# Kernel tuning notes

Measured on AMD Instinct MI355X. Metric: run time of the kernel, lower is better.

The kernel has to match this reference:

```python
import jax, jax.numpy as jnp
import numpy as np

B, L, D, H = 4, 2048, 512, 8
HD = D // H
NEG = -1e9


def setup_inputs() -> dict:
    key = jax.random.key(0)
    ks = jax.random.split(key, 11)
    s = 1.0 / np.sqrt(D)
    inp = {
        "q": jax.random.normal(ks[0], (B, L, D), jnp.float32),
        "k": jax.random.normal(ks[1], (B, L, D), jnp.float32),
        "v": jax.random.normal(ks[2], (B, L, D), jnp.float32),
        "mask": jnp.broadcast_to(jnp.tril(jnp.ones((L, L), jnp.int32)), (B, L, L)),
        "Wq": jax.random.normal(ks[3], (D, D), jnp.float32) * s,
        "bq": jax.random.normal(ks[4], (D,), jnp.float32) * s,
        "Wk": jax.random.normal(ks[5], (D, D), jnp.float32) * s,
        "bk": jax.random.normal(ks[6], (D,), jnp.float32) * s,
        "Wv": jax.random.normal(ks[7], (D, D), jnp.float32) * s,
        "bv": jax.random.normal(ks[8], (D,), jnp.float32) * s,
        "Wo": jax.random.normal(ks[9], (D, D), jnp.float32) * s,
        "bo": jax.random.normal(ks[10], (D,), jnp.float32) * s,
    }
    return inp


def reference(q, k, v, mask, Wq, bq, Wk, bk, Wv, bv, Wo, bo):
    # Linear projections (torch Linear: x @ W.T + b)
    Q = (q @ Wq.T + bq).reshape(B, L, H, HD).transpose(0, 2, 1, 3)  # [B,H,L,hd]
    K = (k @ Wk.T + bk).reshape(B, L, H, HD).transpose(0, 2, 1, 3)
    V = (v @ Wv.T + bv).reshape(B, L, H, HD).transpose(0, 2, 1, 3)
    # scaled dot-product attention with masked_fill(mask==0, -1e9)
    score = jnp.einsum('bhqd,bhkd->bhqk', Q, K) / jnp.sqrt(jnp.float32(HD))
    score = jnp.where(mask[:, None, :, :] == 0, NEG, score)
    attn = jax.nn.softmax(score, axis=-1)
    ctx = jnp.einsum('bhqk,bhkd->bhqd', attn, V)  # [B,H,L,hd]
    ctx = ctx.transpose(0, 2, 1, 3).reshape(B, L, D)
    return ctx @ Wo.T + bo
```

## Files before the change

### kernel.cpp

```cpp
#include <hip/hip_runtime.h>
#include <hip/hip_bf16.h>
#include <math.h>

constexpr int Bc  = 4;
constexpr int Lc  = 2048;
constexpr int Dc  = 512;
constexpr int Hc  = 8;
constexpr int HDc = 64;

constexpr int GK = Dc;
constexpr int BK = 64;

typedef __attribute__((ext_vector_type(8))) short bf16x8;
typedef __attribute__((ext_vector_type(4))) short bf16x4;
typedef __attribute__((ext_vector_type(4))) float f32x4;
typedef __attribute__((ext_vector_type(16))) float f32x16;
typedef __attribute__((ext_vector_type(4))) int i32x4;

static __device__ __forceinline__ short f2bf(float x) {
    __hip_bfloat16 h = __float2bfloat16(x);
    return (short)__builtin_bit_cast(unsigned short, h);
}

static __device__ __forceinline__ int cvtpk_bf16(float lo, float hi) {
    int r;
    asm("v_cvt_pk_bf16_f32 %0, %1, %2" : "=v"(r) : "v"(lo), "v"(hi));
    return r;
}

static __device__ __forceinline__ void gload_lds16(const void* g, void* l) {
    __builtin_amdgcn_global_load_lds(
        (const __attribute__((address_space(1))) void*)g,
        (__attribute__((address_space(3))) void*)l, 16, 0, 0);
}

__global__ __launch_bounds__(256)
void cast_all(const float* __restrict__ q, const float* __restrict__ k,
              const float* __restrict__ v, const float* __restrict__ wq,
              const float* __restrict__ wk, const float* __restrict__ wv,
              const float* __restrict__ wo, short* __restrict__ dst) {
    const size_t i = ((size_t)blockIdx.x * 256 + threadIdx.x) * 8;
    const float* src; size_t off;
    if      (i <  4194304) { src = q;  off = i; }
    else if (i <  8388608) { src = k;  off = i -  4194304; }
    else if (i < 12582912) { src = v;  off = i -  8388608; }
    else if (i < 12845056) { src = wq; off = i - 12582912; }
    else if (i < 13107200) { src = wk; off = i - 12845056; }
    else if (i < 13369344) { src = wv; off = i - 13107200; }
    else                   { src = wo; off = i - 13369344; }
    const float4 a = *(const float4*)(src + off);
    const float4 b = *(const float4*)(src + off + 4);
    bf16x8 o;
    o[0] = f2bf(a.x); o[1] = f2bf(a.y); o[2] = f2bf(a.z); o[3] = f2bf(a.w);
    o[4] = f2bf(b.x); o[5] = f2bf(b.y); o[6] = f2bf(b.z); o[7] = f2bf(b.w);
    *(bf16x8*)(dst + i) = o;
}

template<int BM, int BN, int WMT, int WNT>
__device__ __forceinline__ void gemm_tile(const short* __restrict__ A,
                                          const short* __restrict__ W,
                                          short* As, short* Bs,
                                          f32x4 (&acc)[WMT][WNT],
                                          int m0, int n0) {
    const int tid  = threadIdx.x;
    const int w    = tid >> 6;
    const int lane = tid & 63;
    const int low4 = lane & 15;
    const int quad = lane >> 4;
    const int wm   = w & 1, wn = w >> 1;
    const int lrow = lane >> 3;
    const int lchk = (lane & 7) * 8;

    for (int k0 = 0; k0 < GK; k0 += BK) {
#pragma unroll
        for (int i = 0; i < BM / 32; ++i) {
            const int r0 = i * 32 + w * 8;
            gload_lds16(A + (size_t)(m0 + r0 + lrow) * GK + k0 + lchk, As + r0 * BK);
        }
#pragma unroll
        for (int i = 0; i < BN / 32; ++i) {
            const int r0 = i * 32 + w * 8;
            gload_lds16(W + (size_t)(n0 + r0 + lrow) * GK + k0 + lchk, Bs + r0 * BK);
        }
        __syncthreads();
#pragma unroll
        for (int ks = 0; ks < 2; ++ks) {
            bf16x8 af[WMT], bfr[WNT];
#pragma unroll
            for (int mi = 0; mi < WMT; ++mi)
                af[mi] = *(const bf16x8*)(As + (wm * WMT * 16 + mi * 16 + low4) * BK + ks * 32 + quad * 8);
#pragma unroll
            for (int ni = 0; ni < WNT; ++ni)
                bfr[ni] = *(const bf16x8*)(Bs + (wn * WNT * 16 + ni * 16 + low4) * BK + ks * 32 + quad * 8);
#pragma unroll
            for (int mi = 0; mi < WMT; ++mi)
#pragma unroll
                for (int ni = 0; ni < WNT; ++ni)
                    acc[mi][ni] = __builtin_amdgcn_mfma_f32_16x16x32_bf16(af[mi], bfr[ni], acc[mi][ni], 0, 0, 0);
        }
        __syncthreads();
    }
}

__global__ __launch_bounds__(256)
void qkv_gemm(const short* __restrict__ Xq, const short* __restrict__ Xk,
              const short* __restrict__ Xv, const short* __restrict__ Wcat,
              const float* __restrict__ bq, const float* __restrict__ bk,
              const float* __restrict__ bv,
              short* __restrict__ Qw, short* __restrict__ Kw, short* __restrict__ Vw) {
    __shared__ __align__(16) short Smem[128 * 138];
    short* As = Smem;
    short* Bs = Smem + 8192;
    short* Ts = Smem;

    const int tid = threadIdx.x;
    const int i    = blockIdx.x;
    const int slot = i >> 3;
    const int g    = (i & 7) + 8 * (slot >> 2);
    const int j    = slot & 3;
    const int z    = g >> 6;
    const int m0   = (g & 63) * 128;
    const int n0   = z * 512 + j * 128;

    const short* A    = (z == 0) ? Xq : (z == 1) ? Xk : Xv;
    const float* bias = (z == 0) ? bq : (z == 1) ? bk : bv;

    f32x4 acc[4][4];
#pragma unroll
    for (int mi = 0; mi < 4; ++mi)
#pragma unroll
        for (int ni = 0; ni < 4; ++ni) acc[mi][ni] = (f32x4){0.f, 0.f, 0.f, 0.f};

    gemm_tile<128, 128, 4, 4>(A, Wcat, As, Bs, acc, m0, n0);

    const int lane = tid & 63, w = tid >> 6;
    const int low4 = lane & 15, quad = lane >> 4;
    const int wm = w & 1, wn = w >> 1;

    if (z < 2) {
        short* Y = (z == 0) ? Qw : Kw;
        const float qs = (z == 0) ? 0.18033688f : 1.0f;
#pragma unroll
        for (int mi = 0; mi < 4; ++mi)
#pragma unroll
            for (int ni = 0; ni < 4; ++ni)
#pragma unroll
                for (int r = 0; r < 4; ++r) {
                    const int rowL = wm * 64 + mi * 16 + quad * 4 + r;
                    const int colL = wn * 64 + ni * 16 + low4;
                    const int c    = (n0 & 511) + colL;
                    Ts[rowL * 138 + colL] = f2bf((acc[mi][ni][r] + bias[c]) * qs);
                }
        __syncthreads();
        const int jj = tid & 7;
        const int b = m0 >> 11;
#pragma unroll
        for (int it = 0; it < 8; ++it) {
            const int slot2 = it * 32 + (tid >> 3);
            const int row  = slot2 >> 1, half = slot2 & 1;
            const int c0 = (n0 & 511) + half * 64;
            const int h  = c0 >> 6;
            const int l  = (m0 & 2047) + row;
            short* dst = Y + (((size_t)b * Hc + h) * Lc + l) * HDc + jj * 8;
            *(bf16x8*)dst = *(const bf16x8*)(Ts + row * 138 + half * 64 + jj * 8);
        }
    } else {
#pragma unroll
        for (int mi = 0; mi < 4; ++mi)
#pragma unroll
            for (int ni = 0; ni < 4; ++ni)
#pragma unroll
                for (int r = 0; r < 4; ++r) {
                    const int rowL = wm * 64 + mi * 16 + quad * 4 + r;
                    const int colL = wn * 64 + ni * 16 + low4;
                    const int c    = (n0 + colL) & 511;
                    Ts[colL * 136 + rowL] = f2bf(acc[mi][ni][r] + bias[c]);
                }
        __syncthreads();
        const int hdl = tid >> 1, seg = tid & 1;
        const int c  = (n0 + hdl) & 511;
        const int h  = c >> 6, hd = c & 63;
        const int b  = m0 >> 11, l0 = (m0 & 2047) + seg * 64;
        short* dst = Vw + (((size_t)b * Hc + h) * HDc + hd) * Lc + l0;
        const short* srcT = Ts + hdl * 136 + seg * 64;
#pragma unroll
        for (int jj = 0; jj < 8; ++jj)
            *(bf16x8*)(dst + jj * 8) = *(const bf16x8*)(srcT + jj * 8);
    }
}

__global__ __launch_bounds__(256)
void out_gemm(const short* __restrict__ A, const short* __restrict__ W,
              const float* __restrict__ bias, float* __restrict__ Y) {
    __shared__ __align__(16) float SmemF[64 * 132];
    short* As = (short*)SmemF;
    short* Bs = As + 64 * BK;
    float* Tf = SmemF;

    const int tid = threadIdx.x;
    const int i    = blockIdx.x;
    const int slot = i >> 3;
    const int g    = (i & 7) + 8 * (slot >> 2);
    const int j    = slot & 3;
    const int m0   = g * 64;
    const int n0   = j * 128;

    f32x4 acc[2][4];
#pragma unroll
    for (int mi = 0; mi < 2; ++mi)
#pragma unroll
        for (int ni = 0; ni < 4; ++ni) acc[mi][ni] = (f32x4){0.f, 0.f, 0.f, 0.f};

    gemm_tile<64, 128, 2, 4>(A, W, As, Bs, acc, m0, n0);

    const int lane = tid & 63, w = tid >> 6;
    const int low4 = lane & 15, quad = lane >> 4;
    const int wm = w & 1, wn = w >> 1;
#pragma unroll
    for (int mi = 0; mi < 2; ++mi)
#pragma unroll
        for (int ni = 0; ni < 4; ++ni)
#pragma unroll
            for (int r = 0; r < 4; ++r) {
                const int rowL = wm * 32 + mi * 16 + quad * 4 + r;
                const int colL = wn * 64 + ni * 16 + low4;
                Tf[rowL * 132 + colL] = acc[mi][ni][r] + bias[n0 + colL];
            }
    __syncthreads();

    const int c = (tid & 31) * 4;
#pragma unroll
    for (int p = 0; p < 8; ++p) {
        const int row = p * 8 + (tid >> 5);
        *(float4*)(Y + (size_t)(m0 + row) * Dc + n0 + c) =
            *(const float4*)(Tf + row * 132 + c);
    }
}

__global__ __launch_bounds__(256, 4)
void flash_attn(const short* __restrict__ Qb, const short* __restrict__ Kb,
                const short* __restrict__ VTb, short* __restrict__ ctx) {
    __shared__ __align__(16) short Kf[2][4096];
    __shared__ __align__(16) short Vf[2][4096];

    const int tid  = threadIdx.x;
    const int w    = tid >> 6;
    const int lane = tid & 63;
    const int t31  = lane & 31;
    const int hh   = lane >> 5;
    const int x7   = t31 & 7;
    const int qcol = w & 1;
    const int kh   = w >> 1;

    const int u  = blockIdx.x;
    const int bh = u & 31;
    const int j  = u >> 5;
    const int a  = (j < 16) ? (31 - j) : (j - 16);
    const int n  = a + 1;
    const int q0 = a * 64 + qcol * 32;

    const short* Qg = Qb  + (size_t)bh * Lc * HDc;
    const short* Kg = Kb  + (size_t)bh * Lc * HDc;
    const short* Vg = VTb + (size_t)bh * HDc * Lc;

    const int grow = lane >> 3;
    const int gcol = ((lane & 7) ^ grow) * 8;

    const int bb = bh >> 3, head = bh & 7;
    short* cg = ctx + (size_t)bb * Lc * Dc + (size_t)head * HDc;

#define STAGE(KT_, BUF_)                                                       \
    {                                                                          \
        _Pragma("unroll")                                                      \
        for (int p = 0; p < 2; ++p) {                                          \
            const int ii = w + 4 * p;                                          \
            gload_lds16(Kg + (size_t)((KT_) + ii * 8 + grow) * HDc + gcol,     \
                        &Kf[BUF_][ii * 512]);                                  \
            gload_lds16(Vg + (size_t)(ii * 8 + grow) * Lc + (KT_) + gcol,      \
                        &Vf[BUF_][ii * 512]);                                  \
        }                                                                      \
    }

    bf16x8 qa[4];
#pragma unroll
    for (int hc = 0; hc < 4; ++hc)
        qa[hc] = *(const bf16x8*)(Qg + (size_t)(q0 + t31) * HDc + hc * 16 + hh * 8);

    STAGE(0, 0);
    asm volatile("s_waitcnt vmcnt(0)" ::: "memory");
    __builtin_amdgcn_sched_barrier(0);
    __builtin_amdgcn_s_barrier();

    f32x16 o0, o1;
#pragma unroll
    for (int i = 0; i < 16; ++i) { o0[i] = 0.f; o1[i] = 0.f; }
    float lps = 0.f;

    for (int t = 0; t < n; ++t) {
        const int buf = t & 1;
        if (t + 1 < n) STAGE((t + 1) * 64, buf ^ 1);

        const bool lastT = (t == a);
        if (!(lastT && qcol == 0 && kh == 1)) {
            f32x16 s;
#pragma unroll
            for (int i = 0; i < 16; ++i) s[i] = 0.f;
            const short* kfb = Kf[buf];
#pragma unroll
            for (int hc = 0; hc < 4; ++hc) {
                const int cb = ((hc * 2 + hh) ^ x7) << 3;
                const bf16x8 kfr = *(const bf16x8*)(kfb + (kh * 32 + t31) * 64 + cb);
                s = __builtin_amdgcn_mfma_f32_32x32x16_bf16(kfr, qa[hc], s, 0, 0, 0);
            }

            if (lastT && !(qcol == 1 && kh == 0)) {
                const int qv  = q0 + t31;
                const int kb0 = t * 64 + kh * 32 + 4 * hh;
#pragma unroll
                for (int r = 0; r < 16; ++r) {
                    const int kl = kb0 + (r & 3) + 8 * (r >> 2);
                    const float p = (kl <= qv) ? exp2f(s[r]) : 0.f;
                    lps += p; s[r] = p;
                }
            } else {
#pragma unroll
                for (int r = 0; r < 16; ++r) {
                    const float p = exp2f(s[r]);
                    lps += p; s[r] = p;
                }
            }

            const short* vfb = Vf[buf];
#pragma unroll
            for (int kc = 0; kc < 2; ++kc) {
                const int g = 8 * kc;
                int u0 = cvtpk_bf16(s[g],     s[g + 1]);
                int u1 = cvtpk_bf16(s[g + 2], s[g + 3]);
                int v0 = cvtpk_bf16(s[g + 4], s[g + 5]);
                int v1 = cvtpk_bf16(s[g + 6], s[g + 7]);
                asm volatile("v_permlane32_swap_b32 %0, %1" : "+v"(u0), "+v"(v0));
                asm volatile("v_permlane32_swap_b32 %0, %1" : "+v"(u1), "+v"(v1));
                i32x4 pw; pw[0] = u0; pw[1] = u1; pw[2] = v0; pw[3] = v1;
                const bf16x8 pa = __builtin_bit_cast(bf16x8, pw);

                const int cbv = ((kh * 4 + kc * 2 + hh) ^ x7) << 3;
                const bf16x8 vf0 = *(const bf16x8*)(vfb + t31 * 64 + cbv);
                const bf16x8 vf1 = *(const bf16x8*)(vfb + (32 + t31) * 64 + cbv);
                o0 = __builtin_amdgcn_mfma_f32_32x32x16_bf16(pa, vf0, o0, 0, 0, 0);
                o1 = __builtin_amdgcn_mfma_f32_32x32x16_bf16(pa, vf1, o1, 0, 0, 0);
            }
        }

        asm volatile("s_waitcnt vmcnt(0)" ::: "memory");
        __builtin_amdgcn_sched_barrier(0);
        __builtin_amdgcn_s_barrier();
    }

    lps += __shfl_xor(lps, 32, 64);

    float* CbX = (qcol == 0) ? (float*)&Kf[1][0] : (float*)&Vf[1][0];
    float* ClX = (float*)&Kf[0][0] + qcol * 64;

    if (kh == 1) {
#pragma unroll
        for (int jj = 0; jj < 4; ++jj) {
            f32x4 a0 = {o0[4 * jj], o0[4 * jj + 1], o0[4 * jj + 2], o0[4 * jj + 3]};
            f32x4 a1 = {o1[4 * jj], o1[4 * jj + 1], o1[4 * jj + 2], o1[4 * jj + 3]};
            *(f32x4*)&CbX[lane * 32 + jj * 4]      = a0;
            *(f32x4*)&CbX[lane * 32 + 16 + jj * 4] = a1;
        }
        ClX[lane] = lps;
    }
    __syncthreads();
    if (kh == 0) {
        lps += ClX[lane];
#pragma unroll
        for (int jj = 0; jj < 4; ++jj) {
            const f32x4 a0 = *(const f32x4*)&CbX[lane * 32 + jj * 4];
            const f32x4 a1 = *(const f32x4*)&CbX[lane * 32 + 16 + jj * 4];
#pragma unroll
            for (int e = 0; e < 4; ++e) {
                o0[4 * jj + e] += a0[e];
                o1[4 * jj + e] += a1[e];
            }
        }
        const float inv = 1.f / lps;
#pragma unroll
        for (int r = 0; r < 16; ++r) {
            const int qloc = (r & 3) + 8 * (r >> 2) + 4 * hh;
            const float iq = __shfl(inv, qloc, 64);
            short* row = cg + (size_t)(q0 + qloc) * Dc;
            row[t31]      = f2bf(o0[r] * iq);
            row[32 + t31] = f2bf(o1[r] * iq);
        }
    }
#undef STAGE
}

extern "C" void kernel_launch(void* const* d_in, const int* in_sizes, int n_in,
                              void* d_out, int out_size, void* d_ws, size_t ws_size,
                              hipStream_t stream) {
    const float* q  = (const float*)d_in[0];
    const float* k  = (const float*)d_in[1];
    const float* v  = (const float*)d_in[2];
    const float* Wq = (const float*)d_in[4];
    const float* bq = (const float*)d_in[5];
    const float* Wk = (const float*)d_in[6];
    const float* bk = (const float*)d_in[7];
    const float* Wv = (const float*)d_in[8];
    const float* bv = (const float*)d_in[9];
    const float* Wo = (const float*)d_in[10];
    const float* bo = (const float*)d_in[11];
    float* out = (float*)d_out;

    const size_t per = (size_t)Bc * Lc * Dc;
    const size_t wsz = (size_t)Dc * Dc;
    short* Xq   = (short*)d_ws;
    short* Xk   = Xq + per;
    short* Xv   = Xk + per;
    short* Wcat = Xv + per;
    short* Wob  = Wcat + 3 * wsz;
    short* Qw   = Wob + wsz;
    short* Kw   = Qw + per;
    short* Vw   = Kw + per;
    short* Cw   = Vw + per;

    cast_all<<<6656, 256, 0, stream>>>(q, k, v, Wq, Wk, Wv, Wo, Xq);

    qkv_gemm<<<768, 256, 0, stream>>>(Xq, Xk, Xv, Wcat,
                                      bq, bk, bv, Qw, Kw, Vw);

    flash_attn<<<1024, 256, 0, stream>>>(Qw, Kw, Vw, Cw);

    out_gemm<<<512, 256, 0, stream>>>(Cw, Wob, bo, out);
}
```

Measured before the change: 223.0 us.

## Split long causal query tiles across two blocks with atomic-counter merge

The flash attention grid grows from 1024 to 1536 blocks. Query tiles 16-31 with the longest causal key ranges are each split into two halves of KV tiles. Each half writes unnormalized partial O and row sums to a workspace, and the second block to finish (chosen with an atomic counter) merges them and writes the normalized output. The goal is to balance load and shorten the tail from the longest tiles. In exchange it adds fp32 workspace traffic, threadfences, an atomic, and a memset launch.

```diff
diff --git a/kernel.cpp b/kernel.cpp
--- a/kernel.cpp
+++ b/kernel.cpp
@@ -239,7 +239,9 @@
 
 __global__ __launch_bounds__(256, 4)
 void flash_attn(const short* __restrict__ Qb, const short* __restrict__ Kb,
-                const short* __restrict__ VTb, short* __restrict__ ctx) {
+                const short* __restrict__ VTb, short* __restrict__ ctx,
+                float* __restrict__ Ows, float* __restrict__ Lws,
+                int* __restrict__ cnt) {
     __shared__ __align__(16) short Kf[2][4096];
     __shared__ __align__(16) short Vf[2][4096];
 
@@ -254,9 +256,24 @@
 
     const int u  = blockIdx.x;
     const int bh = u & 31;
-    const int j  = u >> 5;
-    const int a  = (j < 16) ? (31 - j) : (j - 16);
-    const int n  = a + 1;
+    const int e  = u >> 5;
+
+    int a, t0, t1, c;
+    bool split;
+    if (e < 32) {
+        a = 31 - (e >> 1);
+        const int n = a + 1;
+        const int h = (n + 1) >> 1;
+        c  = e & 1;
+        t0 = c ? h : 0;
+        t1 = c ? n : h;
+        split = true;
+    } else {
+        a = 47 - e;
+        c = 0; t0 = 0; t1 = a + 1;
+        split = false;
+    }
+    const int nt = t1 - t0;
     const int q0 = a * 64 + qcol * 32;
 
     const short* Qg = Qb  + (size_t)bh * Lc * HDc;
@@ -286,7 +303,7 @@
     for (int hc = 0; hc < 4; ++hc)
         qa[hc] = *(const bf16x8*)(Qg + (size_t)(q0 + t31) * HDc + hc * 16 + hh * 8);
 
-    STAGE(0, 0);
+    STAGE(t0 * 64, 0);
     asm volatile("s_waitcnt vmcnt(0)" ::: "memory");
     __builtin_amdgcn_sched_barrier(0);
     __builtin_amdgcn_s_barrier();
@@ -296,11 +313,12 @@
     for (int i = 0; i < 16; ++i) { o0[i] = 0.f; o1[i] = 0.f; }
     float lps = 0.f;
 
-    for (int t = 0; t < n; ++t) {
+    for (int t = 0; t < nt; ++t) {
         const int buf = t & 1;
-        if (t + 1 < n) STAGE((t + 1) * 64, buf ^ 1);
-
-        const bool lastT = (t == a);
+        const int tg  = t0 + t;
+        if (t + 1 < nt) STAGE((tg + 1) * 64, buf ^ 1);
+
+        const bool lastT = (tg == a);
         if (!(lastT && qcol == 0 && kh == 1)) {
             f32x16 s;
 #pragma unroll
@@ -315,7 +333,7 @@
 
             if (lastT && !(qcol == 1 && kh == 0)) {
                 const int qv  = q0 + t31;
-                const int kb0 = t * 64 + kh * 32 + 4 * hh;
+                const int kb0 = tg * 64 + kh * 32 + 4 * hh;
 #pragma unroll
                 for (int r = 0; r < 16; ++r) {
                     const int kl = kb0 + (r & 3) + 8 * (r >> 2);
@@ -358,8 +376,9 @@
 
     lps += __shfl_xor(lps, 32, 64);
 
-    float* CbX = (qcol == 0) ? (float*)&Kf[1][0] : (float*)&Vf[1][0];
-    float* ClX = (float*)&Kf[0][0] + qcol * 64;
+    float* CbX  = (qcol == 0) ? (float*)&Kf[1][0] : (float*)&Vf[1][0];
+    float* ClX  = (float*)&Kf[0][0] + qcol * 64;
+    int* flagp  = (int*)&Kf[0][0] + 192;
 
     if (kh == 1) {
 #pragma unroll
@@ -379,11 +398,49 @@
             const f32x4 a0 = *(const f32x4*)&CbX[lane * 32 + jj * 4];
             const f32x4 a1 = *(const f32x4*)&CbX[lane * 32 + 16 + jj * 4];
 #pragma unroll
-            for (int e = 0; e < 4; ++e) {
-                o0[4 * jj + e] += a0[e];
-                o1[4 * jj + e] += a1[e];
-            }
-        }
+            for (int ee = 0; ee < 4; ++ee) {
+                o0[4 * jj + ee] += a0[ee];
+                o1[4 * jj + ee] += a1[ee];
+            }
+        }
+    }
+
+    if (!split) {
+        if (kh == 0) {
+            const float inv = 1.f / lps;
+#pragma unroll
+            for (int r = 0; r < 16; ++r) {
+                const int qloc = (r & 3) + 8 * (r >> 2) + 4 * hh;
+                const float iq = __shfl(inv, qloc, 64);
+                short* row = cg + (size_t)(q0 + qloc) * Dc;
+                row[t31]      = f2bf(o0[r] * iq);
+                row[32 + t31] = f2bf(o1[r] * iq);
+            }
+        }
+        return;
+    }
+
+    const int slot = (bh << 4) | (a - 16);
+    if (kh == 0) {
+        float* dst = Ows + ((size_t)(slot * 2 + c) << 12) + qcol * 2048 + lane * 32;
+#pragma unroll
+        for (int r = 0; r < 16; ++r) { dst[r] = o0[r]; dst[16 + r] = o1[r]; }
+        if (hh == 0) Lws[(slot * 2 + c) * 64 + qcol * 32 + t31] = lps;
+    }
+    __threadfence();
+    __syncthreads();
+    if (tid == 0) *flagp = atomicAdd(&cnt[slot], 1);
+    __syncthreads();
+    if (*flagp == 0) return;
+
+    __threadfence();
+    if (kh == 0) {
+        const float* Po = Ows + ((size_t)(slot * 2 + (1 - c)) << 12)
+                        + qcol * 2048 + lane * 32;
+#pragma unroll
+        for (int r = 0; r < 16; ++r) { o0[r] += Po[r]; o1[r] += Po[16 + r]; }
+        lps += Lws[(slot * 2 + (1 - c)) * 64 + qcol * 32 + t31];
+
         const float inv = 1.f / lps;
 #pragma unroll
         for (int r = 0; r < 16; ++r) {
@@ -424,13 +481,18 @@
     short* Kw   = Qw + per;
     short* Vw   = Kw + per;
     short* Cw   = Vw + per;
+    float* Ows  = (float*)(Cw + per);
+    float* Lws  = Ows + (size_t)1024 * 4096;
+    int*   cnt  = (int*)(Lws + 1024 * 64);
+
+    hipMemsetAsync(cnt, 0, 512 * sizeof(int), stream);
 
     cast_all<<<6656, 256, 0, stream>>>(q, k, v, Wq, Wk, Wv, Wo, Xq);
 
     qkv_gemm<<<768, 256, 0, stream>>>(Xq, Xk, Xv, Wcat,
                                       bq, bk, bv, Qw, Kw, Vw);
 
-    flash_attn<<<1024, 256, 0, stream>>>(Qw, Kw, Vw, Cw);
+    flash_attn<<<1536, 256, 0, stream>>>(Qw, Kw, Vw, Cw, Ows, Lws, cnt);
 
     out_gemm<<<512, 256, 0, stream>>>(Cw, Wob, bo, out);
 }
```

Measured after the change: 460.3 us. 2.06x slower.

## Load K/V fragments directly from global memory instead of LDS double-buffering

Applied to the files above, without the earlier changes.

Removes the double-buffered LDS staging of K and V tiles, along with the per-iteration vmcnt wait and block barrier, in the flash attention loop. Each wave now loads its K and V MFMA fragments straight from global memory, relying on L1/L2 caching for the reuse across waves. LDS is kept only for the final cross-wave reduction. This drops synchronisation and LDS traffic but adds redundant global loads and exposes their latency with no prefetch.

```diff
diff --git a/kernel.cpp b/kernel.cpp
--- a/kernel.cpp
+++ b/kernel.cpp
@@ -240,15 +240,14 @@
 __global__ __launch_bounds__(256, 4)
 void flash_attn(const short* __restrict__ Qb, const short* __restrict__ Kb,
                 const short* __restrict__ VTb, short* __restrict__ ctx) {
-    __shared__ __align__(16) short Kf[2][4096];
-    __shared__ __align__(16) short Vf[2][4096];
+    __shared__ __align__(16) float CbS[2][2048];
+    __shared__ float ClS[2][64];
 
     const int tid  = threadIdx.x;
     const int w    = tid >> 6;
     const int lane = tid & 63;
     const int t31  = lane & 31;
     const int hh   = lane >> 5;
-    const int x7   = t31 & 7;
     const int qcol = w & 1;
     const int kh   = w >> 1;
 
@@ -263,103 +262,82 @@
     const short* Kg = Kb  + (size_t)bh * Lc * HDc;
     const short* Vg = VTb + (size_t)bh * HDc * Lc;
 
-    const int grow = lane >> 3;
-    const int gcol = ((lane & 7) ^ grow) * 8;
-
     const int bb = bh >> 3, head = bh & 7;
     short* cg = ctx + (size_t)bb * Lc * Dc + (size_t)head * HDc;
 
-#define STAGE(KT_, BUF_)                                                       \
-    {                                                                          \
-        _Pragma("unroll")                                                      \
-        for (int p = 0; p < 2; ++p) {                                          \
-            const int ii = w + 4 * p;                                          \
-            gload_lds16(Kg + (size_t)((KT_) + ii * 8 + grow) * HDc + gcol,     \
-                        &Kf[BUF_][ii * 512]);                                  \
-            gload_lds16(Vg + (size_t)(ii * 8 + grow) * Lc + (KT_) + gcol,      \
-                        &Vf[BUF_][ii * 512]);                                  \
-        }                                                                      \
-    }
-
     bf16x8 qa[4];
 #pragma unroll
     for (int hc = 0; hc < 4; ++hc)
         qa[hc] = *(const bf16x8*)(Qg + (size_t)(q0 + t31) * HDc + hc * 16 + hh * 8);
 
-    STAGE(0, 0);
-    asm volatile("s_waitcnt vmcnt(0)" ::: "memory");
-    __builtin_amdgcn_sched_barrier(0);
-    __builtin_amdgcn_s_barrier();
-
     f32x16 o0, o1;
 #pragma unroll
     for (int i = 0; i < 16; ++i) { o0[i] = 0.f; o1[i] = 0.f; }
     float lps = 0.f;
 
+    const short* krow = Kg + (size_t)(kh * 32 + t31) * HDc + hh * 8;
+    const short* vr0  = Vg + (size_t)t31 * Lc        + kh * 32 + hh * 8;
+    const short* vr1  = Vg + (size_t)(32 + t31) * Lc + kh * 32 + hh * 8;
+
     for (int t = 0; t < n; ++t) {
-        const int buf = t & 1;
-        if (t + 1 < n) STAGE((t + 1) * 64, buf ^ 1);
-
         const bool lastT = (t == a);
-        if (!(lastT && qcol == 0 && kh == 1)) {
-            f32x16 s;
-#pragma unroll
-            for (int i = 0; i < 16; ++i) s[i] = 0.f;
-            const short* kfb = Kf[buf];
-#pragma unroll
-            for (int hc = 0; hc < 4; ++hc) {
-                const int cb = ((hc * 2 + hh) ^ x7) << 3;
-                const bf16x8 kfr = *(const bf16x8*)(kfb + (kh * 32 + t31) * 64 + cb);
-                s = __builtin_amdgcn_mfma_f32_32x32x16_bf16(kfr, qa[hc], s, 0, 0, 0);
+        if (lastT && qcol == 0 && kh == 1) break;
+
+        const short* kb = krow + (size_t)t * (64 * HDc);
+        bf16x8 kf0 = *(const bf16x8*)(kb);
+        bf16x8 kf1 = *(const bf16x8*)(kb + 16);
+        bf16x8 kf2 = *(const bf16x8*)(kb + 32);
+        bf16x8 kf3 = *(const bf16x8*)(kb + 48);
+        f32x16 s;
+#pragma unroll
+        for (int i = 0; i < 16; ++i) s[i] = 0.f;
+        s = __builtin_amdgcn_mfma_f32_32x32x16_bf16(kf0, qa[0], s, 0, 0, 0);
+        s = __builtin_amdgcn_mfma_f32_32x32x16_bf16(kf1, qa[1], s, 0, 0, 0);
+        s = __builtin_amdgcn_mfma_f32_32x32x16_bf16(kf2, qa[2], s, 0, 0, 0);
+        s = __builtin_amdgcn_mfma_f32_32x32x16_bf16(kf3, qa[3], s, 0, 0, 0);
+
+        if (lastT && !(qcol == 1 && kh == 0)) {
+            const int qv  = q0 + t31;
+            const int kb0 = t * 64 + kh * 32 + 4 * hh;
+#pragma unroll
+            for (int r = 0; r < 16; ++r) {
+                const int kl = kb0 + (r & 3) + 8 * (r >> 2);
+                const float p = (kl <= qv) ? exp2f(s[r]) : 0.f;
+                lps += p; s[r] = p;
             }
-
-            if (lastT && !(qcol == 1 && kh == 0)) {
-                const int qv  = q0 + t31;
-                const int kb0 = t * 64 + kh * 32 + 4 * hh;
-#pragma unroll
-                for (int r = 0; r < 16; ++r) {
-                    const int kl = kb0 + (r & 3) + 8 * (r >> 2);
-                    const float p = (kl <= qv) ? exp2f(s[r]) : 0.f;
-                    lps += p; s[r] = p;
-                }
-            } else {
-#pragma unroll
-                for (int r = 0; r < 16; ++r) {
-                    const float p = exp2f(s[r]);
-                    lps += p; s[r] = p;
-                }
+        } else {
+#pragma unroll
+            for (int r = 0; r < 16; ++r) {
+                const float p = exp2f(s[r]);
+                lps += p; s[r] = p;
             }
-
-            const short* vfb = Vf[buf];
-#pragma unroll
-            for (int kc = 0; kc < 2; ++kc) {
-                const int g = 8 * kc;
-                int u0 = cvtpk_bf16(s[g],     s[g + 1]);
-                int u1 = cvtpk_bf16(s[g + 2], s[g + 3]);
-                int v0 = cvtpk_bf16(s[g + 4], s[g + 5]);
-                int v1 = cvtpk_bf16(s[g + 6], s[g + 7]);
-                asm volatile("v_permlane32_swap_b32 %0, %1" : "+v"(u0), "+v"(v0));
-                asm volatile("v_permlane32_swap_b32 %0, %1" : "+v"(u1), "+v"(v1));
-                i32x4 pw; pw[0] = u0; pw[1] = u1; pw[2] = v0; pw[3] = v1;
-                const bf16x8 pa = __builtin_bit_cast(bf16x8, pw);
-
-                const int cbv = ((kh * 4 + kc * 2 + hh) ^ x7) << 3;
-                const bf16x8 vf0 = *(const bf16x8*)(vfb + t31 * 64 + cbv);
-                const bf16x8 vf1 = *(const bf16x8*)(vfb + (32 + t31) * 64 + cbv);
-                o0 = __builtin_amdgcn_mfma_f32_32x32x16_bf16(pa, vf0, o0, 0, 0, 0);
-                o1 = __builtin_amdgcn_mfma_f32_32x32x16_bf16(pa, vf1, o1, 0, 0, 0);
-            }
-        }
-
-        asm volatile("s_waitcnt vmcnt(0)" ::: "memory");
-        __builtin_amdgcn_sched_barrier(0);
-        __builtin_amdgcn_s_barrier();
+        }
+
+        const short* vb0 = vr0 + t * 64;
+        const short* vb1 = vr1 + t * 64;
+#pragma unroll
+        for (int kc = 0; kc < 2; ++kc) {
+            const int g = 8 * kc;
+            int u0 = cvtpk_bf16(s[g],     s[g + 1]);
+            int u1 = cvtpk_bf16(s[g + 2], s[g + 3]);
+            int v0 = cvtpk_bf16(s[g + 4], s[g + 5]);
+            int v1 = cvtpk_bf16(s[g + 6], s[g + 7]);
+            asm volatile("v_permlane32_swap_b32 %0, %1" : "+v"(u0), "+v"(v0));
+            asm volatile("v_permlane32_swap_b32 %0, %1" : "+v"(u1), "+v"(v1));
+            i32x4 pw; pw[0] = u0; pw[1] = u1; pw[2] = v0; pw[3] = v1;
+            const bf16x8 pa = __builtin_bit_cast(bf16x8, pw);
+
+            const bf16x8 vf0 = *(const bf16x8*)(vb0 + kc * 16);
+            const bf16x8 vf1 = *(const bf16x8*)(vb1 + kc * 16);
+            o0 = __builtin_amdgcn_mfma_f32_32x32x16_bf16(pa, vf0, o0, 0, 0, 0);
+            o1 = __builtin_amdgcn_mfma_f32_32x32x16_bf16(pa, vf1, o1, 0, 0, 0);
+        }
     }
 
     lps += __shfl_xor(lps, 32, 64);
 
-    float* CbX = (qcol == 0) ? (float*)&Kf[1][0] : (float*)&Vf[1][0];
-    float* ClX = (float*)&Kf[0][0] + qcol * 64;
+    float* CbX = CbS[qcol];
+    float* ClX = ClS[qcol];
 
     if (kh == 1) {
 #pragma unroll
@@ -394,7 +372,6 @@
             row[32 + t31] = f2bf(o1[r] * iq);
         }
     }
-#undef STAGE
 }
 
 extern "C" void kernel_launch(void* const* d_in, const int* in_sizes, int n_in,
```

After: 253.4 us. +13.6%, slower.

## Enlarge flash attention query tile to 128 rows with 512-thread blocks

Applied to the files above, without the earlier changes.

Each flash-attention block now covers 128 query rows with 8 waves (4 query columns by 2 key halves) instead of 64 rows with 4 waves. Every staged K/V tile is therefore shared by twice as many query rows, which halves global-to-LDS traffic per query, and the grid shrinks to 512 blocks. Causal skipping is generalised to a per-wave key-range test. The cost is fewer, larger blocks, lower per-CU occupancy flexibility, and more wasted diagonal tiles in which some waves sit idle.

```diff
diff --git a/kernel.cpp b/kernel.cpp
--- a/kernel.cpp
+++ b/kernel.cpp
@@ -237,11 +237,13 @@
     }
 }
 
-__global__ __launch_bounds__(256, 4)
+__global__ __launch_bounds__(512, 2)
 void flash_attn(const short* __restrict__ Qb, const short* __restrict__ Kb,
                 const short* __restrict__ VTb, short* __restrict__ ctx) {
-    __shared__ __align__(16) short Kf[2][4096];
-    __shared__ __align__(16) short Vf[2][4096];
+    __shared__ __align__(16) short Smem[16384];
+    __shared__ float ClS[4][64];
+    short* KfB = Smem;
+    short* VfB = Smem + 8192;
 
     const int tid  = threadIdx.x;
     const int w    = tid >> 6;
@@ -249,15 +251,15 @@
     const int t31  = lane & 31;
     const int hh   = lane >> 5;
     const int x7   = t31 & 7;
-    const int qcol = w & 1;
-    const int kh   = w >> 1;
+    const int qcol = w & 3;
+    const int kh   = w >> 2;
 
     const int u  = blockIdx.x;
     const int bh = u & 31;
     const int j  = u >> 5;
-    const int a  = (j < 16) ? (31 - j) : (j - 16);
-    const int n  = a + 1;
-    const int q0 = a * 64 + qcol * 32;
+    const int a  = (j < 8) ? (15 - j) : (j - 8);
+    const int n  = 2 * a + 2;
+    const int q0 = a * 128 + qcol * 32;
 
     const short* Qg = Qb  + (size_t)bh * Lc * HDc;
     const short* Kg = Kb  + (size_t)bh * Lc * HDc;
@@ -271,14 +273,10 @@
 
 #define STAGE(KT_, BUF_)                                                       \
     {                                                                          \
-        _Pragma("unroll")                                                      \
-        for (int p = 0; p < 2; ++p) {                                          \
-            const int ii = w + 4 * p;                                          \
-            gload_lds16(Kg + (size_t)((KT_) + ii * 8 + grow) * HDc + gcol,     \
-                        &Kf[BUF_][ii * 512]);                                  \
-            gload_lds16(Vg + (size_t)(ii * 8 + grow) * Lc + (KT_) + gcol,      \
-                        &Vf[BUF_][ii * 512]);                                  \
-        }                                                                      \
+        gload_lds16(Kg + (size_t)((KT_) + w * 8 + grow) * HDc + gcol,          \
+                    KfB + (BUF_) * 4096 + w * 512);                            \
+        gload_lds16(Vg + (size_t)(w * 8 + grow) * Lc + (KT_) + gcol,           \
+                    VfB + (BUF_) * 4096 + w * 512);                            \
     }
 
     bf16x8 qa[4];
@@ -300,12 +298,12 @@
         const int buf = t & 1;
         if (t + 1 < n) STAGE((t + 1) * 64, buf ^ 1);
 
-        const bool lastT = (t == a);
-        if (!(lastT && qcol == 0 && kh == 1)) {
+        const int kmin = t * 64 + kh * 32;
+        if (kmin <= q0 + 31) {
             f32x16 s;
 #pragma unroll
             for (int i = 0; i < 16; ++i) s[i] = 0.f;
-            const short* kfb = Kf[buf];
+            const short* kfb = KfB + buf * 4096;
 #pragma unroll
             for (int hc = 0; hc < 4; ++hc) {
                 const int cb = ((hc * 2 + hh) ^ x7) << 3;
@@ -313,9 +311,9 @@
                 s = __builtin_amdgcn_mfma_f32_32x32x16_bf16(kfr, qa[hc], s, 0, 0, 0);
             }
 
-            if (lastT && !(qcol == 1 && kh == 0)) {
+            if (kmin + 31 > q0) {
                 const int qv  = q0 + t31;
-                const int kb0 = t * 64 + kh * 32 + 4 * hh;
+                const int kb0 = kmin + 4 * hh;
 #pragma unroll
                 for (int r = 0; r < 16; ++r) {
                     const int kl = kb0 + (r & 3) + 8 * (r >> 2);
@@ -330,7 +328,7 @@
                 }
             }
 
-            const short* vfb = Vf[buf];
+            const short* vfb = VfB + buf * 4096;
 #pragma unroll
             for (int kc = 0; kc < 2; ++kc) {
                 const int g = 8 * kc;
@@ -358,8 +356,8 @@
 
     lps += __shfl_xor(lps, 32, 64);
 
-    float* CbX = (qcol == 0) ? (float*)&Kf[1][0] : (float*)&Vf[1][0];
-    float* ClX = (float*)&Kf[0][0] + qcol * 64;
+    float* CbX = (float*)Smem + qcol * 2048;
+    float* ClX = ClS[qcol];
 
     if (kh == 1) {
 #pragma unroll
@@ -430,7 +428,7 @@
     qkv_gemm<<<768, 256, 0, stream>>>(Xq, Xk, Xv, Wcat,
                                       bq, bk, bv, Qw, Kw, Vw);
 
-    flash_attn<<<1024, 256, 0, stream>>>(Qw, Kw, Vw, Cw);
+    flash_attn<<<512, 512, 0, stream>>>(Qw, Kw, Vw, Cw);
 
     out_gemm<<<512, 256, 0, stream>>>(Cw, Wob, bo, out);
 }
```

Measured after the change: 231.7 us. 3.9% more time.
